# Optimization experiments

Hardware: AMD Instinct MI355X
Metric: run time of the kernel (lower is better)

Reference implementation:

```python
import jax, jax.numpy as jnp
import numpy as np
from jax.scipy.special import logsumexp

B, L, M, D = 8192, 1024, 128, 2  # batch, hilbert.size, bond dim, local_size
MACHINE_POW = 2


def setup_inputs() -> dict:
    key = jax.random.key(0)
    k1, k2 = jax.random.split(key)
    # configurations in the zero-magnetization sector: each row is a permutation
    # of L//2 zeros and L//2 ones (constrained HomogeneousHilbert)
    base = jnp.tile(jnp.arange(D, dtype=jnp.int32), L // D)  # (L,)
    inputs = jax.vmap(lambda k: jax.random.permutation(k, base))(jax.random.split(k1, B))
    # variational parameters epsilon: (local_size, M, size); centered at 1 so the
    # length-L multiplicative cache chain stays in fp32 range
    epsilon = 1.0 + 0.02 * jax.random.normal(k2, (D, M, L), dtype=jnp.float32)
    return {"inputs": inputs, "epsilon": epsilon}


def _conditionals(inputs, epsilon):
    # inputs: (B, L) int in [0, D); epsilon: (D, M, L)
    Bn, Ln = inputs.shape
    Dn, Mn, _ = epsilon.shape
    half = Ln // 2

    def scan_fun(carry, index):
        cache, n_spins = carry                       # (B, D, M), (B, D)
        prev = inputs[:, (index - 1) % Ln]           # (B,) previous-site state
        params_i = epsilon[:, :, index]              # (D, M)
        # irregular gather: cache[b, prev[b], :]
        gathered = jnp.take_along_axis(cache, prev[:, None, None], axis=1)[:, 0, :]  # (B, M)
        prods = params_i[None, :, :] * gathered[:, None, :]  # (B, D, M)
        log_psi = jnp.sum(prods, axis=-1)            # (B, D) sum over bond dim
        n_spins = jnp.where(index > 0,
                            n_spins + jax.nn.one_hot(prev, Dn, dtype=jnp.int32),
                            n_spins)
        # zero-magnetization renormalization: -inf once a local state is exhausted
        renorm = jnp.log(jnp.heaviside((half - n_spins).astype(log_psi.dtype), 0.0))
        return (prods, n_spins), log_psi + renorm

    cache0 = jnp.ones((Bn, Dn, Mn), epsilon.dtype)
    n0 = jnp.zeros((Bn, Dn), jnp.int32)
    _, log_psi = jax.lax.scan(scan_fun, (cache0, n0), jnp.arange(Ln))
    return jnp.transpose(log_psi, (1, 0, 2))  # (B, L, D)


def reference(inputs, epsilon):
    lp = _conditionals(inputs, epsilon)  # (B, L, D)
    # normalize conditionals over local states (machine_pow = 2)
    lp = lp - (1.0 / MACHINE_POW) * logsumexp(MACHINE_POW * lp, axis=-1, keepdims=True)
    # pick the log-conditional of the actual configuration at each site
    sel = jnp.take_along_axis(lp, inputs[:, :, None], axis=2)[:, :, 0]  # (B, L)
    # n_symm = 1 (default apply_symmetries): symmetrized logsumexp is identity
    return jnp.sum(sel, axis=1)  # (B,) log_psi
```

## Files before the change

### kernel.cpp

```cpp
#include <hip/hip_runtime.h>

typedef unsigned long long u64;
typedef unsigned int uint32;
typedef short short8 __attribute__((ext_vector_type(8)));
typedef float f32x4 __attribute__((ext_vector_type(4)));

#define B_N 8192
#define L_N 1024
#define M_N 128
#define C_N 16
#define CH_N 64
#define HALF_N 512
#define SL 20
#define ROWF (8 * SL)

#define OFF_W    0
#define OFF_R    0x80000
#define OFF_BITS 0x100000
#define OFF_LR   0x208000
#define OFF_RQ   0x248000

__device__ __forceinline__ unsigned short f32_bf16(float f) {
    union { float f; unsigned u; } x; x.f = f;
    unsigned u = x.u + 0x7FFFu + ((x.u >> 16) & 1u);
    return (unsigned short)(u >> 16);
}
__device__ __forceinline__ float bf16lo(uint32 w) {
    union { unsigned u; float f; } x; x.u = w << 16; return x.f;
}
__device__ __forceinline__ float bf16hi(uint32 w) {
    union { unsigned u; float f; } x; x.u = w & 0xFFFF0000u; return x.f;
}

__device__ __forceinline__ float2 pk_fma(float2 a, float2 b, float2 c) {
    float2 d;
    asm("v_pk_fma_f32 %0, %1, %2, %3" : "=v"(d) : "v"(a), "v"(b), "v"(c));
    return d;
}
__device__ __forceinline__ float2 pk_mul(float2 a, float2 b) {
    float2 d;
    asm("v_pk_mul_f32 %0, %1, %2" : "=v"(d) : "v"(a), "v"(b));
    return d;
}

__global__ __launch_bounds__(256) void k_pack(const int* __restrict__ inp, u64* __restrict__ bits) {
    int g = blockIdx.x * 256 + threadIdx.x;
    int v = inp[g];
    u64 m = __ballot(v != 0);
    if ((threadIdx.x & 63) == 0) bits[g >> 6] = m;
}

__global__ __launch_bounds__(64) void k_eps(const float* __restrict__ eps,
        float* __restrict__ w, float* __restrict__ r, unsigned short* __restrict__ lrT) {
    int m = blockIdx.x, lane = threadIdx.x;
    const float* e0 = eps + (size_t)m * L_N + lane * 16;
    const float* e1 = eps + (size_t)(M_N + m) * L_N + lane * 16;
    float a[16], b[16];
    #pragma unroll
    for (int j = 0; j < 16; j += 4) {
        *(float4*)&a[j] = *(const float4*)&e0[j];
        *(float4*)&b[j] = *(const float4*)&e1[j];
    }
    float local = 1.f;
    #pragma unroll
    for (int j = 0; j < 16; ++j) local *= a[j];
    float sc = local;
    #pragma unroll
    for (int d = 1; d < 64; d <<= 1) {
        float up = __shfl_up(sc, d);
        if (lane >= d) sc *= up;
    }
    float prev = __shfl_up(sc, 1);
    float E = (lane == 0) ? 1.f : prev;
    int i0 = lane * 16;
    #pragma unroll
    for (int j = 0; j < 16; ++j) {
        float rat = b[j] / a[j];
        w[(size_t)(i0 + j) * M_N + m] = E * (a[j] - b[j]);
        r[(size_t)(i0 + j) * M_N + m] = rat;
        lrT[(size_t)m * L_N + i0 + j] = f32_bf16(__log2f(rat));
        E *= a[j];
    }
}

__global__ __launch_bounds__(256) void k_slog2(const u64* __restrict__ bits,
        const unsigned short* __restrict__ lrT, unsigned short* __restrict__ Rq) {
    int btile = blockIdx.x;
    int mq = threadIdx.x >> 6, lane = threadIdx.x & 63;
    int col = lane & 15, quad = lane >> 4;
    int b_row = btile * 16 + col;
    const u64* brow = bits + (size_t)b_row * 16;

    f32x4 cum[2];
    cum[0] = (f32x4){0.f, 0.f, 0.f, 0.f};
    cum[1] = (f32x4){0.f, 0.f, 0.f, 0.f};

    for (int c = 0; c < C_N; ++c) {
        #pragma unroll
        for (int mt = 0; mt < 2; ++mt) {
            #pragma unroll
            for (int reg = 0; reg < 4; ++reg) {
                int b = btile * 16 + quad * 4 + reg;
                int m = mq * 32 + mt * 16 + col;
                Rq[((size_t)c * B_N + b) * M_N + m] = f32_bf16(exp2f(cum[mt][reg]));
            }
        }
        u64 wv = brow[c];
        short8 a0, a1;
        #pragma unroll
        for (int j = 0; j < 8; ++j) {
            a0[j] = (short)((((wv >> (quad * 8 + j)) & 1) != 0) ? 0x3F80 : 0);
            a1[j] = (short)((((wv >> (32 + quad * 8 + j)) & 1) != 0) ? 0x3F80 : 0);
        }
        #pragma unroll
        for (int mt = 0; mt < 2; ++mt) {
            int m = mq * 32 + mt * 16 + col;
            const unsigned short* bp = lrT + (size_t)m * L_N + c * 64 + quad * 8;
            union { uint4 u; short8 s; } bf0, bf1;
            bf0.u = *(const uint4*)bp;
            bf1.u = *(const uint4*)(bp + 32);
            cum[mt] = __builtin_amdgcn_mfma_f32_16x16x32_bf16(a0, bf0.s, cum[mt], 0, 0, 0);
            cum[mt] = __builtin_amdgcn_mfma_f32_16x16x32_bf16(a1, bf1.s, cum[mt], 0, 0, 0);
        }
    }
}

__global__ __launch_bounds__(256, 4) void k_main(const u64* __restrict__ bits,
        const float* __restrict__ w, const float* __restrict__ r,
        const unsigned short* __restrict__ Rq, float* __restrict__ out) {
    __shared__ float wbuf[32 * ROWF];
    __shared__ float rbuf[32 * ROWF];
    int c = blockIdx.x & (C_N - 1);
    int bblk = blockIdx.x >> 4;
    int lane = threadIdx.x & 63, wid = threadIdx.x >> 6;
    int s = lane & 7, g = lane >> 3;
    int b0 = bblk * 128 + wid * 32 + g * 4;
    int b_own = b0 + (s & 3);

    float2 R2[4][8];
    #pragma unroll
    for (int nb = 0; nb < 4; ++nb) {
        const uint4* src = (const uint4*)(Rq + ((size_t)c * B_N + (b0 + nb)) * M_N + s * 16);
        #pragma unroll
        for (int u_ = 0; u_ < 2; ++u_) {
            uint4 pv = src[u_];
            R2[nb][u_ * 4 + 0] = make_float2(bf16lo(pv.x), bf16hi(pv.x));
            R2[nb][u_ * 4 + 1] = make_float2(bf16lo(pv.y), bf16hi(pv.y));
            R2[nb][u_ * 4 + 2] = make_float2(bf16lo(pv.z), bf16hi(pv.z));
            R2[nb][u_ * 4 + 3] = make_float2(bf16lo(pv.w), bf16hi(pv.w));
        }
    }
    int n1 = 0;
    for (int k = 0; k < c; ++k) n1 += __popcll(bits[(size_t)b_own * 16 + k]);
    int n0 = c * CH_N - n1;

    float sum = 0.f;
    for (int h = 0; h < 2; ++h) {
        __syncthreads();
        const float4* srcw = (const float4*)(w + ((size_t)c * CH_N + h * 32) * M_N);
        const float4* srcr = (const float4*)(r + ((size_t)c * CH_N + h * 32) * M_N);
        for (int t = threadIdx.x; t < 32 * 32; t += 256) {
            int i = t >> 5, mqd = t & 31;
            int dst = i * ROWF + (mqd >> 2) * SL + (mqd & 3) * 4;
            *(float4*)&wbuf[dst] = srcw[t];
            *(float4*)&rbuf[dst] = srcr[t];
        }
        __syncthreads();

        uint32 wh[4];
        #pragma unroll
        for (int nb = 0; nb < 4; ++nb)
            wh[nb] = (uint32)(bits[(size_t)(b0 + nb) * 16 + c] >> (h * 32));
        uint32 owa = (s & 1) ? wh[1] : wh[0];
        uint32 owb = (s & 1) ? wh[3] : wh[2];
        uint32 ow = (s & 2) ? owb : owa;

        for (int tt = 0; tt < 32; ++tt) {
            int base = tt * ROWF + s * SL;
            const float2* wp = (const float2*)&wbuf[base];
            float2 w2[8];
            #pragma unroll
            for (int j = 0; j < 8; ++j) w2[j] = wp[j];

            float d[4];
            #pragma unroll
            for (int nb = 0; nb < 4; ++nb) {
                float2 acc = pk_mul(R2[nb][0], w2[0]);
                #pragma unroll
                for (int j = 1; j < 8; ++j) acc = pk_fma(R2[nb][j], w2[j], acc);
                d[nb] = acc.x + acc.y;
            }
            #pragma unroll
            for (int nb = 0; nb < 4; ++nb) {
                d[nb] += __shfl_xor(d[nb], 1);
                d[nb] += __shfl_xor(d[nb], 2);
            }
            int sb3 = s & 3;
            float sel = d[0];
            if (sb3 == 1) sel = d[1];
            if (sb3 == 2) sel = d[2];
            if (sb3 == 3) sel = d[3];
            sel += __shfl_xor(sel, 4);
            float Dv = sel;

            int sbit = (ow >> tt) & 1;
            bool valid = (n0 < HALF_N) && (n1 < HALF_N);
            float ad = fabsf(Dv);
            float contr = -fmaxf(sbit ? Dv : -Dv, 0.f)
                          - 0.5f * __logf(1.f + __expf(-2.f * ad));
            sum += valid ? contr : 0.f;
            n1 += sbit; n0 += 1 - sbit;

            const float2* rp = (const float2*)&rbuf[base];
            float2 r2[8];
            #pragma unroll
            for (int j = 0; j < 8; ++j) r2[j] = rp[j];
            #pragma unroll
            for (int nb = 0; nb < 4; ++nb) {
                if ((wh[nb] >> tt) & 1) {
                    #pragma unroll
                    for (int j = 0; j < 8; ++j) R2[nb][j] = pk_mul(R2[nb][j], r2[j]);
                }
            }
        }
    }
    if (s < 4) atomicAdd(&out[b_own], sum);
}

extern "C" void kernel_launch(void* const* d_in, const int* in_sizes, int n_in,
                              void* d_out, int out_size, void* d_ws, size_t ws_size,
                              hipStream_t stream) {
    const int*   inputs  = (const int*)d_in[0];
    const float* epsilon = (const float*)d_in[1];
    float* out = (float*)d_out;

    char* ws = (char*)d_ws;
    float* w_tab  = (float*)(ws + OFF_W);
    float* r_tab  = (float*)(ws + OFF_R);
    u64*   bits   = (u64*)  (ws + OFF_BITS);
    unsigned short* lrT = (unsigned short*)(ws + OFF_LR);
    unsigned short* Rq  = (unsigned short*)(ws + OFF_RQ);

    k_pack<<<(B_N * L_N) / 256, 256, 0, stream>>>(inputs, bits);
    k_eps<<<M_N, 64, 0, stream>>>(epsilon, w_tab, r_tab, lrT);
    hipMemsetAsync(d_out, 0, B_N * sizeof(float), stream);
    k_slog2<<<B_N / 16, 256, 0, stream>>>(bits, lrT, Rq);
    k_main<<<(B_N / 128) * C_N, 256, 0, stream>>>(bits, w_tab, r_tab, Rq, out);
}
```

Baseline: 199.1 us.

## Split k_slog2 across two blocks per tile and use compiler vector ops in k_main

k_slog2 now launches twice as many blocks, each handling half of the bond dimension with one MFMA accumulator per wave instead of two. The goal is more parallelism and fewer live registers in the prefix-sum kernel. In k_main, the inline-asm packed FMA/mul helpers give way to ext_vector_type float2 arithmetic, so the compiler can schedule and fuse the packed ops itself. The trade-off is that the bits row is loaded redundantly per half, and the compiler may not emit v_pk_fma as reliably as the explicit asm did.

```diff
diff --git a/kernel.cpp b/kernel.cpp
--- a/kernel.cpp
+++ b/kernel.cpp
@@ -4,6 +4,7 @@
 typedef unsigned int uint32;
 typedef short short8 __attribute__((ext_vector_type(8)));
 typedef float f32x4 __attribute__((ext_vector_type(4)));
+typedef float f32x2 __attribute__((ext_vector_type(2)));
 
 #define B_N 8192
 #define L_N 1024
@@ -32,17 +33,6 @@
     union { unsigned u; float f; } x; x.u = w & 0xFFFF0000u; return x.f;
 }
 
-__device__ __forceinline__ float2 pk_fma(float2 a, float2 b, float2 c) {
-    float2 d;
-    asm("v_pk_fma_f32 %0, %1, %2, %3" : "=v"(d) : "v"(a), "v"(b), "v"(c));
-    return d;
-}
-__device__ __forceinline__ float2 pk_mul(float2 a, float2 b) {
-    float2 d;
-    asm("v_pk_mul_f32 %0, %1, %2" : "=v"(d) : "v"(a), "v"(b));
-    return d;
-}
-
 __global__ __launch_bounds__(256) void k_pack(const int* __restrict__ inp, u64* __restrict__ bits) {
     int g = blockIdx.x * 256 + threadIdx.x;
     int v = inp[g];
@@ -85,25 +75,22 @@
 
 __global__ __launch_bounds__(256) void k_slog2(const u64* __restrict__ bits,
         const unsigned short* __restrict__ lrT, unsigned short* __restrict__ Rq) {
-    int btile = blockIdx.x;
-    int mq = threadIdx.x >> 6, lane = threadIdx.x & 63;
+    int btile = blockIdx.x >> 1;
+    int half = blockIdx.x & 1;
+    int wid = threadIdx.x >> 6, lane = threadIdx.x & 63;
     int col = lane & 15, quad = lane >> 4;
+    int m = (half * 4 + wid) * 16 + col;
     int b_row = btile * 16 + col;
     const u64* brow = bits + (size_t)b_row * 16;
-
-    f32x4 cum[2];
-    cum[0] = (f32x4){0.f, 0.f, 0.f, 0.f};
-    cum[1] = (f32x4){0.f, 0.f, 0.f, 0.f};
+    const unsigned short* lrow = lrT + (size_t)m * L_N;
+
+    f32x4 cum = (f32x4){0.f, 0.f, 0.f, 0.f};
 
     for (int c = 0; c < C_N; ++c) {
         #pragma unroll
-        for (int mt = 0; mt < 2; ++mt) {
-            #pragma unroll
-            for (int reg = 0; reg < 4; ++reg) {
-                int b = btile * 16 + quad * 4 + reg;
-                int m = mq * 32 + mt * 16 + col;
-                Rq[((size_t)c * B_N + b) * M_N + m] = f32_bf16(exp2f(cum[mt][reg]));
-            }
+        for (int reg = 0; reg < 4; ++reg) {
+            int b = btile * 16 + quad * 4 + reg;
+            Rq[((size_t)c * B_N + b) * M_N + m] = f32_bf16(exp2f(cum[reg]));
         }
         u64 wv = brow[c];
         short8 a0, a1;
@@ -112,16 +99,12 @@
             a0[j] = (short)((((wv >> (quad * 8 + j)) & 1) != 0) ? 0x3F80 : 0);
             a1[j] = (short)((((wv >> (32 + quad * 8 + j)) & 1) != 0) ? 0x3F80 : 0);
         }
-        #pragma unroll
-        for (int mt = 0; mt < 2; ++mt) {
-            int m = mq * 32 + mt * 16 + col;
-            const unsigned short* bp = lrT + (size_t)m * L_N + c * 64 + quad * 8;
-            union { uint4 u; short8 s; } bf0, bf1;
-            bf0.u = *(const uint4*)bp;
-            bf1.u = *(const uint4*)(bp + 32);
-            cum[mt] = __builtin_amdgcn_mfma_f32_16x16x32_bf16(a0, bf0.s, cum[mt], 0, 0, 0);
-            cum[mt] = __builtin_amdgcn_mfma_f32_16x16x32_bf16(a1, bf1.s, cum[mt], 0, 0, 0);
-        }
+        const unsigned short* bp = lrow + c * 64 + quad * 8;
+        union { uint4 u; short8 s; } bf0, bf1;
+        bf0.u = *(const uint4*)bp;
+        bf1.u = *(const uint4*)(bp + 32);
+        cum = __builtin_amdgcn_mfma_f32_16x16x32_bf16(a0, bf0.s, cum, 0, 0, 0);
+        cum = __builtin_amdgcn_mfma_f32_16x16x32_bf16(a1, bf1.s, cum, 0, 0, 0);
     }
 }
 
@@ -137,17 +120,17 @@
     int b0 = bblk * 128 + wid * 32 + g * 4;
     int b_own = b0 + (s & 3);
 
-    float2 R2[4][8];
+    f32x2 R2[4][8];
     #pragma unroll
     for (int nb = 0; nb < 4; ++nb) {
         const uint4* src = (const uint4*)(Rq + ((size_t)c * B_N + (b0 + nb)) * M_N + s * 16);
         #pragma unroll
         for (int u_ = 0; u_ < 2; ++u_) {
             uint4 pv = src[u_];
-            R2[nb][u_ * 4 + 0] = make_float2(bf16lo(pv.x), bf16hi(pv.x));
-            R2[nb][u_ * 4 + 1] = make_float2(bf16lo(pv.y), bf16hi(pv.y));
-            R2[nb][u_ * 4 + 2] = make_float2(bf16lo(pv.z), bf16hi(pv.z));
-            R2[nb][u_ * 4 + 3] = make_float2(bf16lo(pv.w), bf16hi(pv.w));
+            R2[nb][u_ * 4 + 0] = (f32x2){bf16lo(pv.x), bf16hi(pv.x)};
+            R2[nb][u_ * 4 + 1] = (f32x2){bf16lo(pv.y), bf16hi(pv.y)};
+            R2[nb][u_ * 4 + 2] = (f32x2){bf16lo(pv.z), bf16hi(pv.z)};
+            R2[nb][u_ * 4 + 3] = (f32x2){bf16lo(pv.w), bf16hi(pv.w)};
         }
     }
     int n1 = 0;
@@ -177,18 +160,18 @@
 
         for (int tt = 0; tt < 32; ++tt) {
             int base = tt * ROWF + s * SL;
-            const float2* wp = (const float2*)&wbuf[base];
-            float2 w2[8];
+            const f32x2* wp = (const f32x2*)&wbuf[base];
+            f32x2 w2[8];
             #pragma unroll
             for (int j = 0; j < 8; ++j) w2[j] = wp[j];
 
             float d[4];
             #pragma unroll
             for (int nb = 0; nb < 4; ++nb) {
-                float2 acc = pk_mul(R2[nb][0], w2[0]);
+                f32x2 acc = R2[nb][0] * w2[0];
                 #pragma unroll
-                for (int j = 1; j < 8; ++j) acc = pk_fma(R2[nb][j], w2[j], acc);
-                d[nb] = acc.x + acc.y;
+                for (int j = 1; j < 8; ++j) acc += R2[nb][j] * w2[j];
+                d[nb] = acc[0] + acc[1];
             }
             #pragma unroll
             for (int nb = 0; nb < 4; ++nb) {
@@ -211,15 +194,15 @@
             sum += valid ? contr : 0.f;
             n1 += sbit; n0 += 1 - sbit;
 
-            const float2* rp = (const float2*)&rbuf[base];
-            float2 r2[8];
+            const f32x2* rp = (const f32x2*)&rbuf[base];
+            f32x2 r2[8];
             #pragma unroll
             for (int j = 0; j < 8; ++j) r2[j] = rp[j];
             #pragma unroll
             for (int nb = 0; nb < 4; ++nb) {
                 if ((wh[nb] >> tt) & 1) {
                     #pragma unroll
-                    for (int j = 0; j < 8; ++j) R2[nb][j] = pk_mul(R2[nb][j], r2[j]);
+                    for (int j = 0; j < 8; ++j) R2[nb][j] *= r2[j];
                 }
             }
         }
@@ -244,6 +227,6 @@
     k_pack<<<(B_N * L_N) / 256, 256, 0, stream>>>(inputs, bits);
     k_eps<<<M_N, 64, 0, stream>>>(epsilon, w_tab, r_tab, lrT);
     hipMemsetAsync(d_out, 0, B_N * sizeof(float), stream);
-    k_slog2<<<B_N / 16, 256, 0, stream>>>(bits, lrT, Rq);
+    k_slog2<<<(B_N / 16) * 2, 256, 0, stream>>>(bits, lrT, Rq);
     k_main<<<(B_N / 128) * C_N, 256, 0, stream>>>(bits, w_tab, r_tab, Rq, out);
 }
```

Result: no change. 196.8 us (-1.1%).
